# Optimization experiments

Measured on AMD Instinct MI355X. Metric: run time of the kernel, lower is better.

## Reference

```python
import jax, jax.numpy as jnp
import numpy as np

H = 16
D_MODEL = 1024
D_K = D_MODEL // H  # 64, must equal embeddim


def setup_inputs() -> dict:
    key = jax.random.key(0)
    ks = jax.random.split(key, 20)
    B, S, D = 4, 1024, D_MODEL
    s = 0.02
    inp = {
        'query': jax.random.normal(ks[0], (B, S, D), jnp.float32),
        'key':   jax.random.normal(ks[1], (B, S, D), jnp.float32),
        'value': jax.random.normal(ks[2], (B, S, D), jnp.float32),
        'mask':  jnp.ones((B, S, S), jnp.int32),
        # four d_model x d_model projections (q, k, v, out)
        'wq': jax.random.normal(ks[3], (D, D), jnp.float32) * s, 'bq': jnp.zeros((D,), jnp.float32),
        'wk': jax.random.normal(ks[4], (D, D), jnp.float32) * s, 'bk': jnp.zeros((D,), jnp.float32),
        'wv': jax.random.normal(ks[5], (D, D), jnp.float32) * s, 'bv': jnp.zeros((D,), jnp.float32),
        'wo': jax.random.normal(ks[6], (D, D), jnp.float32) * s, 'bo': jnp.zeros((D,), jnp.float32),
        # per-head (embeddim=64) linears
        'spatial_w': jax.random.normal(ks[7], (D_K, D_K), jnp.float32) * s, 'spatial_b': jnp.zeros((D_K,), jnp.float32),
        'qproj_w':   jax.random.normal(ks[8], (D_K, D_K), jnp.float32) * s, 'qproj_b':   jnp.zeros((D_K,), jnp.float32),
        'kproj_w':   jax.random.normal(ks[9], (D_K, D_K), jnp.float32) * s, 'kproj_b':   jnp.zeros((D_K,), jnp.float32),
        'vlin_w':    jax.random.normal(ks[10], (D_K, D_K), jnp.float32) * s, 'vlin_b':    jnp.zeros((D_K,), jnp.float32),
        # channel_linear: Linear(1, 64)
        'chan_w': jax.random.normal(ks[11], (1, D_K), jnp.float32) * s, 'chan_b': jnp.zeros((D_K,), jnp.float32),
    }
    return inp


def reference(query, key, value, mask,
              wq, bq, wk, bk, wv, bv, wo, bo,
              spatial_w, spatial_b, qproj_w, qproj_b,
              kproj_w, kproj_b, vlin_w, vlin_b, chan_w, chan_b):
    B, S, D = query.shape
    # project and split heads -> [B, H, S, D_K]
    def heads(x, w, b):
        return (x @ w + b).reshape(B, S, H, D_K).transpose(0, 2, 1, 3)
    q = heads(query, wq, bq)
    k = heads(key, wk, bk)
    v = heads(value, wv, bv)

    q = jax.nn.elu(q @ spatial_w + spatial_b)
    q_refine = q @ qproj_w + qproj_b
    # channel gate: mean over channels -> Linear(1,64) -> matmul with raw key
    alpha = q_refine.mean(-1, keepdims=True) @ chan_w + chan_b        # [B,H,S,64]
    gate = jax.nn.sigmoid(jnp.einsum('bhqe,bhke->bhqk', alpha, k))    # [B,H,S,S]

    k2 = jax.nn.elu(k @ kproj_w + kproj_b)
    scores = jnp.einsum('bhqe,bhke->bhqk', q, k2) / jnp.sqrt(jnp.asarray(D_K, q.dtype))
    scores = scores * gate
    scores = jnp.where(mask[:, None] == 0, jnp.asarray(-1e9, scores.dtype), scores)
    p_attn = jax.nn.softmax(scores, axis=-1)

    v2 = jax.nn.elu(v @ vlin_w + vlin_b)
    x = jnp.einsum('bhqk,bhke->bhqe', p_attn, v2)                     # [B,H,S,64]
    x = x.transpose(0, 2, 1, 3).reshape(B, S, H * D_K)
    return x @ wo + bo
```

## Files before the change

### kernel.cpp

```cpp
#include <hip/hip_runtime.h>
#include <math.h>

#define D_MODEL 1024
#define NH 16
#define DK 64
#define S_LEN 1024
#define BATCH 4
#define MROWS (BATCH * S_LEN)

typedef short bf16x8 __attribute__((ext_vector_type(8)));
typedef float f32x4 __attribute__((ext_vector_type(4)));
typedef unsigned short u16;

__device__ __forceinline__ float elu1(float x) {
    return x > 0.f ? x : (expf(x) - 1.f);
}

__device__ __forceinline__ u16 f2bf(float f) {
    union { float f; unsigned u; } v; v.f = f;
    unsigned u = v.u;
    return (u16)((u + 0x7fffu + ((u >> 16) & 1u)) >> 16);
}

__device__ __forceinline__ u16 f2bf_fast(float f) {
    union { float f; unsigned u; } v; v.f = f;
    return (u16)((v.u + 0x8000u) >> 16);
}

__device__ __forceinline__ void async16(const void* g, void* l) {
    __builtin_amdgcn_global_load_lds(
        (const __attribute__((address_space(1))) unsigned int*)g,
        (__attribute__((address_space(3))) unsigned int*)l,
        16, 0, 0);
}

__global__ __launch_bounds__(256) void cast_wt(
    const float* __restrict__ wq, const float* __restrict__ wk,
    const float* __restrict__ wv, const float* __restrict__ wo,
    u16* __restrict__ WT)
{
    __shared__ float T[64][65];
    const int z = blockIdx.z;
    const float* W = (z == 0) ? wq : ((z == 1) ? wk : ((z == 2) ? wv : wo));
    u16* O = WT + (size_t)z * D_MODEL * D_MODEL;
    const int tid = threadIdx.x;
    const int k0 = blockIdx.y * 64, n0 = blockIdx.x * 64;
    const int r = tid >> 4, c4 = (tid & 15) * 4;
    #pragma unroll
    for (int p = 0; p < 4; p++) {
        float4 v = *(const float4*)&W[(size_t)(k0 + r + p * 16) * D_MODEL + n0 + c4];
        T[r + p * 16][c4 + 0] = v.x; T[r + p * 16][c4 + 1] = v.y;
        T[r + p * 16][c4 + 2] = v.z; T[r + p * 16][c4 + 3] = v.w;
    }
    __syncthreads();
    #pragma unroll
    for (int p = 0; p < 4; p++) {
        const int i = r + p * 16;
        ushort4 o4;
        o4.x = f2bf(T[c4 + 0][i]); o4.y = f2bf(T[c4 + 1][i]);
        o4.z = f2bf(T[c4 + 2][i]); o4.w = f2bf(T[c4 + 3][i]);
        *(ushort4*)&O[(size_t)(n0 + i) * D_MODEL + k0 + c4] = o4;
    }
}

__global__ __launch_bounds__(256) void cast_x(
    const float* __restrict__ Xq, const float* __restrict__ Xk,
    const float* __restrict__ Xv, u16* __restrict__ Xb)
{
    const int z = blockIdx.y;
    const float* X = (z == 0) ? Xq : ((z == 1) ? Xk : Xv);
    u16* O = Xb + (size_t)z * MROWS * D_MODEL;
    const size_t i = ((size_t)blockIdx.x * 256 + threadIdx.x) * 8;
    float4 a = *(const float4*)&X[i];
    float4 b = *(const float4*)&X[i + 4];
    ushort4 o0, o1;
    o0.x = f2bf(a.x); o0.y = f2bf(a.y); o0.z = f2bf(a.z); o0.w = f2bf(a.w);
    o1.x = f2bf(b.x); o1.y = f2bf(b.y); o1.z = f2bf(b.z); o1.w = f2bf(b.w);
    *(ushort4*)&O[i] = o0;
    *(ushort4*)&O[i + 4] = o1;
}

__global__ __launch_bounds__(256) void mask_pack(
    const int* __restrict__ mask, unsigned long long* __restrict__ Mb)
{
    const int gw = (blockIdx.x * 256 + threadIdx.x) >> 6;
    const int lane = threadIdx.x & 63;
    for (int i = 0; i < 64; i++) {
        const size_t w = (size_t)gw * 64 + i;
        int v = mask[w * 64 + lane];
        unsigned long long bits = __ballot(v != 0);
        if (lane == 0) Mb[w] = bits;
    }
}

__global__ __launch_bounds__(256) void proj_fused(
    const u16* __restrict__ Xq, const u16* __restrict__ Xk, const u16* __restrict__ Xv,
    const u16* __restrict__ WTq, const u16* __restrict__ WTk, const u16* __restrict__ WTv,
    const float* __restrict__ bq, const float* __restrict__ bk, const float* __restrict__ bv,
    const float* __restrict__ spatial_w, const float* __restrict__ spatial_b,
    const float* __restrict__ qproj_w, const float* __restrict__ qproj_b,
    const float* __restrict__ kproj_w, const float* __restrict__ kproj_b,
    const float* __restrict__ vlin_w, const float* __restrict__ vlin_b,
    const float* __restrict__ chan_w, const float* __restrict__ chan_b,
    u16* __restrict__ Qh, u16* __restrict__ K2, u16* __restrict__ V2t,
    float* __restrict__ mB, float* __restrict__ uB, float* __restrict__ vB)
{
    __shared__ __align__(16) u16 smem[10752];
    __shared__ float auxA[64];
    __shared__ float auxS;

    u16* As = smem;
    u16* Bs = smem + 4096;
    u16* W2t = smem + 6144;

    const int z = blockIdx.z;
    const u16* X = (z == 0) ? Xq : ((z == 1) ? Xk : Xv);
    const u16* WT = (z == 0) ? WTq : ((z == 1) ? WTk : WTv);
    const float* B1 = (z == 0) ? bq : ((z == 1) ? bk : bv);
    const float* W2 = (z == 0) ? spatial_w : ((z == 1) ? kproj_w : vlin_w);
    const float* B2 = (z == 0) ? spatial_b : ((z == 1) ? kproj_b : vlin_b);

    const int tid = threadIdx.x;
    const int wave = tid >> 6, lane = tid & 63;
    const int col = lane & 15, quad = lane >> 4;
    const int r0 = blockIdx.x * 128;
    const int hh = blockIdx.y;
    const int n0 = hh * 64;

    #pragma unroll
    for (int p = 0; p < 4; p++) {
        int idx = p * 256 + tid;
        int f = idx >> 4, e4 = (idx & 15) * 4;
        float4 w4 = *(const float4*)&W2[f * 64 + e4];
        W2t[(e4 + 0) * 72 + f] = f2bf(w4.x);
        W2t[(e4 + 1) * 72 + f] = f2bf(w4.y);
        W2t[(e4 + 2) * 72 + f] = f2bf(w4.z);
        W2t[(e4 + 3) * 72 + f] = f2bf(w4.w);
    }
    if (z == 0) {
        {
            int row = tid >> 2, part = tid & 3;
            float s = 0.f;
            for (int e = part * 16; e < part * 16 + 16; e++) s += qproj_w[row * 64 + e];
            s += __shfl_xor(s, 1);
            s += __shfl_xor(s, 2);
            if (part == 0) auxA[row] = s * (1.f / 64.f);
        }
        if (tid < 64) {
            float s = qproj_b[tid];
            #pragma unroll
            for (int m = 1; m < 64; m <<= 1) s += __shfl_xor(s, m);
            if (tid == 0) auxS = s * (1.f / 64.f);
        }
    }

    const int srow = lane >> 2;
    const int sg = ((lane & 3) ^ ((lane >> 3) & 3)) * 8;

    const u16* ap = X + (size_t)(r0 + wave * 32 + srow) * D_MODEL + sg;
    u16* adst0 = As + (wave * 32) * 32;
    u16* adst1 = As + (wave * 32 + 16) * 32;
    const u16* bp = WT + (size_t)(n0 + wave * 16 + srow) * D_MODEL + sg;
    u16* bdst = Bs + wave * 16 * 32;

    f32x4 acc[2][4];
    #pragma unroll
    for (int i = 0; i < 2; i++)
        #pragma unroll
        for (int j = 0; j < 4; j++)
            acc[i][j] = (f32x4){0.f, 0.f, 0.f, 0.f};

    const int gsw = (quad ^ ((col >> 1) & 3)) * 8;

    for (int k0 = 0; k0 < D_MODEL; k0 += 32) {
        if (k0) __syncthreads();
        async16(ap + k0, adst0);
        async16(ap + (size_t)16 * D_MODEL + k0, adst1);
        async16(bp + k0, bdst);
        __syncthreads();
        const u16* Abase = As + (wave * 32 + col) * 32 + gsw;
        const u16* Bbase = Bs + col * 32 + gsw;
        bf16x8 af[2], bfr[4];
        #pragma unroll
        for (int mi = 0; mi < 2; mi++) af[mi] = *(const bf16x8*)(Abase + mi * 512);
        #pragma unroll
        for (int ni = 0; ni < 4; ni++) bfr[ni] = *(const bf16x8*)(Bbase + ni * 512);
        #pragma unroll
        for (int mi = 0; mi < 2; mi++)
            #pragma unroll
            for (int ni = 0; ni < 4; ni++)
                acc[mi][ni] = __builtin_amdgcn_mfma_f32_16x16x32_bf16(af[mi], bfr[ni], acc[mi][ni], 0, 0, 0);
    }

    float b1v[4];
    #pragma unroll
    for (int ni = 0; ni < 4; ni++) b1v[ni] = B1[n0 + ni * 16 + col];

    const int rbase = r0 + wave * 32;
    const int b = r0 >> 10;
    const int s0 = (r0 & 1023) + wave * 32;
    const size_t svecbase = ((size_t)b * NH + hh) * S_LEN;

    if (z == 1) {
        float cw[4], cb[4];
        #pragma unroll
        for (int ni = 0; ni < 4; ni++) { cw[ni] = chan_w[ni * 16 + col]; cb[ni] = chan_b[ni * 16 + col]; }
        #pragma unroll
        for (int mi = 0; mi < 2; mi++)
            #pragma unroll
            for (int r = 0; r < 4; r++) {
                float su = 0.f, sv = 0.f;
                #pragma unroll
                for (int ni = 0; ni < 4; ni++) {
                    float p = acc[mi][ni][r] + b1v[ni];
                    su += p * cw[ni];
                    sv += p * cb[ni];
                }
                su += __shfl_xor(su, 1); su += __shfl_xor(su, 2);
                su += __shfl_xor(su, 4); su += __shfl_xor(su, 8);
                sv += __shfl_xor(sv, 1); sv += __shfl_xor(sv, 2);
                sv += __shfl_xor(sv, 4); sv += __shfl_xor(sv, 8);
                if (col == 0) {
                    const size_t idx = svecbase + s0 + mi * 16 + quad * 4 + r;
                    uB[idx] = su;
                    vB[idx] = sv;
                }
            }
    }

    __syncthreads();

    u16* Pchunk = smem + wave * 1536;
    bf16x8 bf2r[4][2];
    #pragma unroll
    for (int ni = 0; ni < 4; ni++) {
        bf2r[ni][0] = *(const bf16x8*)&W2t[(ni * 16 + col) * 72 + quad * 8];
        bf2r[ni][1] = *(const bf16x8*)&W2t[(ni * 16 + col) * 72 + 32 + quad * 8];
    }
    float qs[2][4][4];
    #pragma unroll
    for (int mi = 0; mi < 2; mi++) {
        #pragma unroll
        for (int ni = 0; ni < 4; ni++)
            #pragma unroll
            for (int r = 0; r < 4; r++)
                Pchunk[(quad * 4 + r) * 72 + ni * 16 + col] = f2bf(acc[mi][ni][r] + b1v[ni]);
        __builtin_amdgcn_s_waitcnt(0xc07f);
        __builtin_amdgcn_sched_barrier(0);
        bf16x8 a0 = *(const bf16x8*)&Pchunk[col * 72 + quad * 8];
        bf16x8 a1 = *(const bf16x8*)&Pchunk[col * 72 + 32 + quad * 8];
        __builtin_amdgcn_s_waitcnt(0xc07f);
        __builtin_amdgcn_sched_barrier(0);
        #pragma unroll
        for (int ni = 0; ni < 4; ni++) {
            f32x4 c = (f32x4){0.f, 0.f, 0.f, 0.f};
            c = __builtin_amdgcn_mfma_f32_16x16x32_bf16(a0, bf2r[ni][0], c, 0, 0, 0);
            c = __builtin_amdgcn_mfma_f32_16x16x32_bf16(a1, bf2r[ni][1], c, 0, 0, 0);
            const float bb = B2[ni * 16 + col];
            #pragma unroll
            for (int r = 0; r < 4; r++) qs[mi][ni][r] = elu1(c[r] + bb);
        }
    }

    if (z == 0) {
        float aw[4];
        #pragma unroll
        for (int ni = 0; ni < 4; ni++) aw[ni] = auxA[ni * 16 + col];
        #pragma unroll
        for (int mi = 0; mi < 2; mi++)
            #pragma unroll
            for (int r = 0; r < 4; r++) {
                float pm = 0.f;
                #pragma unroll
                for (int ni = 0; ni < 4; ni++) pm += qs[mi][ni][r] * aw[ni];
                pm += __shfl_xor(pm, 1); pm += __shfl_xor(pm, 2);
                pm += __shfl_xor(pm, 4); pm += __shfl_xor(pm, 8);
                if (col == 0)
                    mB[svecbase + s0 + mi * 16 + quad * 4 + r] = pm + auxS;
            }
        #pragma unroll
        for (int mi = 0; mi < 2; mi++)
            #pragma unroll
            for (int ni = 0; ni < 4; ni++)
                #pragma unroll
                for (int r = 0; r < 4; r++)
                    Qh[(size_t)(rbase + mi * 16 + quad * 4 + r) * D_MODEL
                       + n0 + ni * 16 + col] = f2bf(qs[mi][ni][r] * 0.125f);
    } else if (z == 1) {
        #pragma unroll
        for (int mi = 0; mi < 2; mi++)
            #pragma unroll
            for (int ni = 0; ni < 4; ni++)
                #pragma unroll
                for (int r = 0; r < 4; r++)
                    K2[(size_t)(rbase + mi * 16 + quad * 4 + r) * D_MODEL
                       + n0 + ni * 16 + col] = f2bf(qs[mi][ni][r]);
    } else {
        u16* Tb = W2t;
        __syncthreads();
        #pragma unroll
        for (int p = 0; p < 2; p++) {
            if ((wave >> 1) == p) {
                const int sloc = (wave & 1) * 32;
                #pragma unroll
                for (int mi = 0; mi < 2; mi++)
                    #pragma unroll
                    for (int ni = 0; ni < 4; ni++)
                        #pragma unroll
                        for (int r = 0; r < 4; r++)
                            Tb[(ni * 16 + col) * 72 + sloc + mi * 16 + quad * 4 + r] =
                                f2bf(qs[mi][ni][r]);
            }
            __syncthreads();
            {
                const int d = tid >> 2, seg = tid & 3;
                u16* dst = V2t + (((size_t)b * NH + hh) * DK + d) * S_LEN
                         + (r0 & 1023) + p * 64 + seg * 16;
                *(uint4*)dst = *(const uint4*)&Tb[d * 72 + seg * 16];
                *(uint4*)(dst + 8) = *(const uint4*)&Tb[d * 72 + seg * 16 + 8];
            }
            if (p == 0) __syncthreads();
        }
    }
}

__global__ __launch_bounds__(256) void attn_mfma(
    const u16* __restrict__ Qh, const u16* __restrict__ K2h, const u16* __restrict__ V2t,
    const float* __restrict__ Mq, const float* __restrict__ Uk, const float* __restrict__ Vk,
    const unsigned long long* __restrict__ Mb, u16* __restrict__ X)
{
    __shared__ u16 K2s[64][72];
    __shared__ u16 V2s[64][72];
    __shared__ u16 Ps[4][16][72];

    const int tid = threadIdx.x;
    const int wave = tid >> 6, lane = tid & 63;
    const int col = lane & 15, quad = lane >> 4;

    const int f = blockIdx.x;
    const int o = (f & 7) * 128 + (f >> 3);
    const int q0 = (o & 15) * 64;
    const int h = (o >> 4) & 15;
    const int b = o >> 8;

    const size_t hb = ((size_t)(b * NH + h)) * S_LEN * DK;
    const size_t sb = ((size_t)(b * NH + h)) * S_LEN;

    bf16x8 qf0, qf1;
    {
        const u16* qp = Qh + (size_t)(b * S_LEN + q0 + wave * 16 + col) * D_MODEL + h * 64 + quad * 8;
        qf0 = *(const bf16x8*)qp;
        qf1 = *(const bf16x8*)(qp + 32);
    }
    float mqv[4];
    #pragma unroll
    for (int r = 0; r < 4; r++)
        mqv[r] = Mq[sb + q0 + wave * 16 + quad * 4 + r];

    const int srow = tid >> 2, sseg = tid & 3;
    const u16* ksrc = K2h + (size_t)(b * S_LEN + srow) * D_MODEL + h * 64 + sseg * 16;
    const u16* vsrc = V2t + hb + (size_t)srow * S_LEN + sseg * 16;
    const unsigned long long* mbase = Mb
        + ((size_t)b * S_LEN + q0 + wave * 16 + quad * 4) * (S_LEN / 64);
    const unsigned msel0 = 1u << col, msel1 = msel0 << 16;

    uint4 ka = *(const uint4*)(ksrc);
    uint4 kb = *(const uint4*)(ksrc + 8);
    uint4 va = *(const uint4*)(vsrc);
    uint4 vb = *(const uint4*)(vsrc + 8);
    float ku[4], kv[4];
    unsigned long long wm[4];
    #pragma unroll
    for (int nb = 0; nb < 4; nb++) {
        ku[nb] = Uk[sb + nb * 16 + col];
        kv[nb] = Vk[sb + nb * 16 + col];
    }
    #pragma unroll
    for (int r = 0; r < 4; r++) wm[r] = mbase[r * 16];

    float psum[4] = {0.f, 0.f, 0.f, 0.f};
    f32x4 o4[4];
    #pragma unroll
    for (int nb = 0; nb < 4; nb++) o4[nb] = (f32x4){0.f, 0.f, 0.f, 0.f};

    for (int t = 0; t < 16; t++) {
        *(uint4*)&K2s[srow][sseg * 16]     = ka;
        *(uint4*)&K2s[srow][sseg * 16 + 8] = kb;
        *(uint4*)&V2s[srow][sseg * 16]     = va;
        *(uint4*)&V2s[srow][sseg * 16 + 8] = vb;
        __syncthreads();

        if (t < 15) {
            const int k1 = (t + 1) * 64;
            const u16* ks = ksrc + (size_t)k1 * D_MODEL;
            const u16* vs = vsrc + k1;
            ka = *(const uint4*)(ks);
            kb = *(const uint4*)(ks + 8);
            va = *(const uint4*)(vs);
            vb = *(const uint4*)(vs + 8);
        }

        __builtin_amdgcn_s_setprio(1);
        f32x4 sc[4];
        #pragma unroll
        for (int nb = 0; nb < 4; nb++) {
            bf16x8 b0 = *(const bf16x8*)&K2s[nb * 16 + col][quad * 8];
            bf16x8 b1 = *(const bf16x8*)&K2s[nb * 16 + col][32 + quad * 8];
            f32x4 c = (f32x4){0.f, 0.f, 0.f, 0.f};
            c = __builtin_amdgcn_mfma_f32_16x16x32_bf16(qf0, b0, c, 0, 0, 0);
            c = __builtin_amdgcn_mfma_f32_16x16x32_bf16(qf1, b1, c, 0, 0, 0);
            sc[nb] = c;
        }
        __builtin_amdgcn_s_setprio(0);

        #pragma unroll
        for (int nb = 0; nb < 4; nb++) {
            #pragma unroll
            for (int r = 0; r < 4; r++) {
                float e = __expf(-(mqv[r] * ku[nb] + kv[nb]));
                float g = __builtin_amdgcn_rcpf(1.f + e);
                float sv = sc[nb][r] * g;
                const unsigned bits = (nb < 2) ? (unsigned)wm[r]
                                               : (unsigned)(wm[r] >> 32);
                sv = (bits & ((nb & 1) ? msel1 : msel0)) ? sv : -30.f;
                float p = __expf(sv);
                psum[r] += p;
                Ps[wave][quad * 4 + r][nb * 16 + col] = f2bf_fast(p);
            }
        }
        if (t < 15) {
            const int k1 = (t + 1) * 64;
            #pragma unroll
            for (int nb = 0; nb < 4; nb++) {
                ku[nb] = Uk[sb + k1 + nb * 16 + col];
                kv[nb] = Vk[sb + k1 + nb * 16 + col];
            }
            #pragma unroll
            for (int r = 0; r < 4; r++) wm[r] = mbase[r * 16 + t + 1];
        }
        __builtin_amdgcn_s_waitcnt(0xc07f);
        __builtin_amdgcn_sched_barrier(0);
        bf16x8 a0 = *(const bf16x8*)&Ps[wave][col][quad * 8];
        bf16x8 a1 = *(const bf16x8*)&Ps[wave][col][32 + quad * 8];

        __builtin_amdgcn_s_setprio(1);
        #pragma unroll
        for (int nb = 0; nb < 4; nb++) {
            bf16x8 b0 = *(const bf16x8*)&V2s[nb * 16 + col][quad * 8];
            bf16x8 b1 = *(const bf16x8*)&V2s[nb * 16 + col][32 + quad * 8];
            o4[nb] = __builtin_amdgcn_mfma_f32_16x16x32_bf16(a0, b0, o4[nb], 0, 0, 0);
            o4[nb] = __builtin_amdgcn_mfma_f32_16x16x32_bf16(a1, b1, o4[nb], 0, 0, 0);
        }
        __builtin_amdgcn_s_setprio(0);
        __syncthreads();
    }

    #pragma unroll
    for (int r = 0; r < 4; r++) {
        float t = psum[r];
        t += __shfl_xor(t, 1);
        t += __shfl_xor(t, 2);
        t += __shfl_xor(t, 4);
        t += __shfl_xor(t, 8);
        float inv = __builtin_amdgcn_rcpf(t);
        u16* xp = X + (size_t)(b * S_LEN + q0 + wave * 16 + quad * 4 + r) * D_MODEL + h * 64 + col;
        #pragma unroll
        for (int nb = 0; nb < 4; nb++)
            xp[nb * 16] = f2bf_fast(o4[nb][r] * inv);
    }
}

__global__ __launch_bounds__(256) void out_gemm(
    const u16* __restrict__ A, const u16* __restrict__ WT,
    const float* __restrict__ bias, float* __restrict__ C)
{
    __shared__ u16 As[64 * 32];
    __shared__ u16 Bs[64 * 32];

    const int tid = threadIdx.x;
    const int wave = tid >> 6, lane = tid & 63;
    const int col = lane & 15, quad = lane >> 4;
    const int r0 = blockIdx.x * 64, n0 = blockIdx.y * 64;

    const int sg = ((lane & 3) ^ ((lane >> 3) & 3)) * 8;
    const u16* ap = A + (size_t)(r0 + wave * 16 + (lane >> 2)) * D_MODEL + sg;
    const u16* bp = WT + (size_t)(n0 + wave * 16 + (lane >> 2)) * D_MODEL + sg;
    u16* adst = As + wave * 16 * 32;
    u16* bdst = Bs + wave * 16 * 32;

    f32x4 acc[4];
    #pragma unroll
    for (int j = 0; j < 4; j++) acc[j] = (f32x4){0.f, 0.f, 0.f, 0.f};

    const int gsw = (quad ^ ((col >> 1) & 3)) * 8;

    for (int k0 = 0; k0 < D_MODEL; k0 += 32) {
        if (k0) __syncthreads();
        async16(ap + k0, adst);
        async16(bp + k0, bdst);
        __syncthreads();
        const u16* Ab = As + (wave * 16 + col) * 32 + gsw;
        const u16* Bb = Bs + col * 32 + gsw;
        bf16x8 af = *(const bf16x8*)Ab;
        bf16x8 bfr[4];
        #pragma unroll
        for (int ni = 0; ni < 4; ni++) bfr[ni] = *(const bf16x8*)(Bb + ni * 512);
        #pragma unroll
        for (int ni = 0; ni < 4; ni++)
            acc[ni] = __builtin_amdgcn_mfma_f32_16x16x32_bf16(af, bfr[ni], acc[ni], 0, 0, 0);
    }

    #pragma unroll
    for (int ni = 0; ni < 4; ni++) {
        const int gr = r0 + wave * 16 + quad * 4;
        const int gc = n0 + ni * 16 + col;
        const float bb = bias[gc];
        #pragma unroll
        for (int r = 0; r < 4; r++)
            C[(size_t)(gr + r) * D_MODEL + gc] = acc[ni][r] + bb;
    }
}

extern "C" void kernel_launch(void* const* d_in, const int* in_sizes, int n_in,
                              void* d_out, int out_size, void* d_ws, size_t ws_size,
                              hipStream_t stream) {
    (void)in_sizes; (void)n_in; (void)out_size; (void)ws_size;
    const float* query = (const float*)d_in[0];
    const float* key_  = (const float*)d_in[1];
    const float* value = (const float*)d_in[2];
    const int*   mask  = (const int*)d_in[3];
    const float* wq = (const float*)d_in[4];  const float* bq = (const float*)d_in[5];
    const float* wk = (const float*)d_in[6];  const float* bk = (const float*)d_in[7];
    const float* wv = (const float*)d_in[8];  const float* bv = (const float*)d_in[9];
    const float* wo = (const float*)d_in[10]; const float* bo = (const float*)d_in[11];
    const float* spatial_w = (const float*)d_in[12]; const float* spatial_b = (const float*)d_in[13];
    const float* qproj_w   = (const float*)d_in[14]; const float* qproj_b   = (const float*)d_in[15];
    const float* kproj_w   = (const float*)d_in[16]; const float* kproj_b   = (const float*)d_in[17];
    const float* vlin_w    = (const float*)d_in[18]; const float* vlin_b    = (const float*)d_in[19];
    const float* chan_w    = (const float*)d_in[20]; const float* chan_b    = (const float*)d_in[21];
    float* out = (float*)d_out;

    char* ws = (char*)d_ws;
    u16* Qh  = (u16*)ws;
    u16* K2  = (u16*)(ws + ((size_t)8  << 20));
    u16* Xb  = (u16*)(ws + ((size_t)16 << 20));
    u16* WT  = (u16*)(ws + ((size_t)24 << 20));
    u16* V2t = (u16*)(ws + ((size_t)32 << 20));
    float* mB = (float*)(ws + ((size_t)40 << 20));
    float* uB = mB + (size_t)BATCH * NH * S_LEN;
    float* vB = uB + (size_t)BATCH * NH * S_LEN;
    unsigned long long* Mbits = (unsigned long long*)(ws + ((size_t)41 << 20));
    u16* Xbf = (u16*)(ws + ((size_t)42 << 20));
    const size_t WSZ = (size_t)D_MODEL * D_MODEL;
    const size_t XSZ = (size_t)MROWS * D_MODEL;

    cast_wt<<<dim3(16, 16, 4), 256, 0, stream>>>(wq, wk, wv, wo, WT);
    cast_x<<<dim3(MROWS * D_MODEL / 2048, 3), 256, 0, stream>>>(query, key_, value, Xbf);
    mask_pack<<<dim3(256), 256, 0, stream>>>(mask, Mbits);
    proj_fused<<<dim3(32, 16, 3), 256, 0, stream>>>(Xbf, Xbf + XSZ, Xbf + 2 * XSZ,
        WT, WT + WSZ, WT + 2 * WSZ, bq, bk, bv,
        spatial_w, spatial_b, qproj_w, qproj_b, kproj_w, kproj_b,
        vlin_w, vlin_b, chan_w, chan_b,
        Qh, K2, V2t, mB, uB, vB);
    attn_mfma<<<dim3(1024), 256, 0, stream>>>(Qh, K2, V2t, mB, uB, vB, Mbits, Xb);
    out_gemm<<<dim3(64, 16), 256, 0, stream>>>(Xb, WT + 3 * WSZ, bo, out);
}
```

Measured before the change: 306.1 us.

## Enlarge GEMM tiles in projection and output kernels, widen mask packing parallelism

The fused projection kernel now computes a 128x128 tile covering two heads per block (each wave handles 64x64), halving the grid in y and doubling the reuse of each A tile. The V transpose is restructured to stage both heads in shared memory and write with wider stores. The output GEMM moves from 64x64 to 128x64 tiles, and mask packing gets 8x more blocks, with each wavefront issuing 8 independent loads before its ballots. The cost is more accumulator registers and shared memory per block, which lowers occupancy, and fewer blocks for the GEMMs.

```diff
diff --git a/kernel.cpp b/kernel.cpp
--- a/kernel.cpp
+++ b/kernel.cpp
@@ -85,11 +85,14 @@
 {
     const int gw = (blockIdx.x * 256 + threadIdx.x) >> 6;
     const int lane = threadIdx.x & 63;
-    for (int i = 0; i < 64; i++) {
-        const size_t w = (size_t)gw * 64 + i;
-        int v = mask[w * 64 + lane];
-        unsigned long long bits = __ballot(v != 0);
-        if (lane == 0) Mb[w] = bits;
+    int v[8];
+    #pragma unroll
+    for (int i = 0; i < 8; i++)
+        v[i] = mask[((size_t)gw + (size_t)i * 8192) * 64 + lane];
+    #pragma unroll
+    for (int i = 0; i < 8; i++) {
+        unsigned long long bits = __ballot(v[i] != 0);
+        if (lane == 0) Mb[(size_t)gw + (size_t)i * 8192] = bits;
     }
 }
 
@@ -105,13 +108,13 @@
     u16* __restrict__ Qh, u16* __restrict__ K2, u16* __restrict__ V2t,
     float* __restrict__ mB, float* __restrict__ uB, float* __restrict__ vB)
 {
-    __shared__ __align__(16) u16 smem[10752];
+    __shared__ __align__(16) u16 smem[17408];
     __shared__ float auxA[64];
     __shared__ float auxS;
 
     u16* As = smem;
     u16* Bs = smem + 4096;
-    u16* W2t = smem + 6144;
+    u16* W2t = smem + 8192;
 
     const int z = blockIdx.z;
     const u16* X = (z == 0) ? Xq : ((z == 1) ? Xk : Xv);
@@ -123,9 +126,10 @@
     const int tid = threadIdx.x;
     const int wave = tid >> 6, lane = tid & 63;
     const int col = lane & 15, quad = lane >> 4;
+    const int wr = wave >> 1, wc = wave & 1;
     const int r0 = blockIdx.x * 128;
-    const int hh = blockIdx.y;
-    const int n0 = hh * 64;
+    const int hp = blockIdx.y * 2 + wc;
+    const int n0 = blockIdx.y * 128;
 
     #pragma unroll
     for (int p = 0; p < 4; p++) {
@@ -158,14 +162,13 @@
     const int sg = ((lane & 3) ^ ((lane >> 3) & 3)) * 8;
 
     const u16* ap = X + (size_t)(r0 + wave * 32 + srow) * D_MODEL + sg;
-    u16* adst0 = As + (wave * 32) * 32;
-    u16* adst1 = As + (wave * 32 + 16) * 32;
-    const u16* bp = WT + (size_t)(n0 + wave * 16 + srow) * D_MODEL + sg;
-    u16* bdst = Bs + wave * 16 * 32;
-
-    f32x4 acc[2][4];
-    #pragma unroll
-    for (int i = 0; i < 2; i++)
+    const u16* bp = WT + (size_t)(n0 + wave * 32 + srow) * D_MODEL + sg;
+    u16* adst0 = As + (wave * 32) * 32;  u16* adst1 = adst0 + 512;
+    u16* bdst0 = Bs + (wave * 32) * 32;  u16* bdst1 = bdst0 + 512;
+
+    f32x4 acc[4][4];
+    #pragma unroll
+    for (int i = 0; i < 4; i++)
         #pragma unroll
         for (int j = 0; j < 4; j++)
             acc[i][j] = (f32x4){0.f, 0.f, 0.f, 0.f};
@@ -176,17 +179,18 @@
         if (k0) __syncthreads();
         async16(ap + k0, adst0);
         async16(ap + (size_t)16 * D_MODEL + k0, adst1);
-        async16(bp + k0, bdst);
+        async16(bp + k0, bdst0);
+        async16(bp + (size_t)16 * D_MODEL + k0, bdst1);
         __syncthreads();
-        const u16* Abase = As + (wave * 32 + col) * 32 + gsw;
-        const u16* Bbase = Bs + col * 32 + gsw;
-        bf16x8 af[2], bfr[4];
-        #pragma unroll
-        for (int mi = 0; mi < 2; mi++) af[mi] = *(const bf16x8*)(Abase + mi * 512);
+        const u16* Abase = As + (wr * 64 + col) * 32 + gsw;
+        const u16* Bbase = Bs + (wc * 64 + col) * 32 + gsw;
+        bf16x8 af[4], bfr[4];
+        #pragma unroll
+        for (int mi = 0; mi < 4; mi++) af[mi] = *(const bf16x8*)(Abase + mi * 512);
         #pragma unroll
         for (int ni = 0; ni < 4; ni++) bfr[ni] = *(const bf16x8*)(Bbase + ni * 512);
         #pragma unroll
-        for (int mi = 0; mi < 2; mi++)
+        for (int mi = 0; mi < 4; mi++)
             #pragma unroll
             for (int ni = 0; ni < 4; ni++)
                 acc[mi][ni] = __builtin_amdgcn_mfma_f32_16x16x32_bf16(af[mi], bfr[ni], acc[mi][ni], 0, 0, 0);
@@ -194,19 +198,19 @@
 
     float b1v[4];
     #pragma unroll
-    for (int ni = 0; ni < 4; ni++) b1v[ni] = B1[n0 + ni * 16 + col];
-
-    const int rbase = r0 + wave * 32;
+    for (int ni = 0; ni < 4; ni++) b1v[ni] = B1[hp * 64 + ni * 16 + col];
+
+    const int rbase = r0 + wr * 64;
     const int b = r0 >> 10;
-    const int s0 = (r0 & 1023) + wave * 32;
-    const size_t svecbase = ((size_t)b * NH + hh) * S_LEN;
+    const int s0 = (r0 & 1023) + wr * 64;
+    const size_t svecbase = ((size_t)b * NH + hp) * S_LEN;
 
     if (z == 1) {
         float cw[4], cb[4];
         #pragma unroll
         for (int ni = 0; ni < 4; ni++) { cw[ni] = chan_w[ni * 16 + col]; cb[ni] = chan_b[ni * 16 + col]; }
         #pragma unroll
-        for (int mi = 0; mi < 2; mi++)
+        for (int mi = 0; mi < 4; mi++)
             #pragma unroll
             for (int r = 0; r < 4; r++) {
                 float su = 0.f, sv = 0.f;
@@ -237,9 +241,9 @@
         bf2r[ni][0] = *(const bf16x8*)&W2t[(ni * 16 + col) * 72 + quad * 8];
         bf2r[ni][1] = *(const bf16x8*)&W2t[(ni * 16 + col) * 72 + 32 + quad * 8];
     }
-    float qs[2][4][4];
-    #pragma unroll
-    for (int mi = 0; mi < 2; mi++) {
+    float qs[4][4][4];
+    #pragma unroll
+    for (int mi = 0; mi < 4; mi++) {
         #pragma unroll
         for (int ni = 0; ni < 4; ni++)
             #pragma unroll
@@ -267,7 +271,7 @@
         #pragma unroll
         for (int ni = 0; ni < 4; ni++) aw[ni] = auxA[ni * 16 + col];
         #pragma unroll
-        for (int mi = 0; mi < 2; mi++)
+        for (int mi = 0; mi < 4; mi++)
             #pragma unroll
             for (int r = 0; r < 4; r++) {
                 float pm = 0.f;
@@ -279,47 +283,45 @@
                     mB[svecbase + s0 + mi * 16 + quad * 4 + r] = pm + auxS;
             }
         #pragma unroll
-        for (int mi = 0; mi < 2; mi++)
+        for (int mi = 0; mi < 4; mi++)
             #pragma unroll
             for (int ni = 0; ni < 4; ni++)
                 #pragma unroll
                 for (int r = 0; r < 4; r++)
                     Qh[(size_t)(rbase + mi * 16 + quad * 4 + r) * D_MODEL
-                       + n0 + ni * 16 + col] = f2bf(qs[mi][ni][r] * 0.125f);
+                       + hp * 64 + ni * 16 + col] = f2bf(qs[mi][ni][r] * 0.125f);
     } else if (z == 1) {
         #pragma unroll
-        for (int mi = 0; mi < 2; mi++)
+        for (int mi = 0; mi < 4; mi++)
             #pragma unroll
             for (int ni = 0; ni < 4; ni++)
                 #pragma unroll
                 for (int r = 0; r < 4; r++)
                     K2[(size_t)(rbase + mi * 16 + quad * 4 + r) * D_MODEL
-                       + n0 + ni * 16 + col] = f2bf(qs[mi][ni][r]);
+                       + hp * 64 + ni * 16 + col] = f2bf(qs[mi][ni][r]);
     } else {
-        u16* Tb = W2t;
         __syncthreads();
-        #pragma unroll
-        for (int p = 0; p < 2; p++) {
-            if ((wave >> 1) == p) {
-                const int sloc = (wave & 1) * 32;
-                #pragma unroll
-                for (int mi = 0; mi < 2; mi++)
-                    #pragma unroll
-                    for (int ni = 0; ni < 4; ni++)
-                        #pragma unroll
-                        for (int r = 0; r < 4; r++)
-                            Tb[(ni * 16 + col) * 72 + sloc + mi * 16 + quad * 4 + r] =
-                                f2bf(qs[mi][ni][r]);
+        u16* Tb = smem + wc * 8704;
+        #pragma unroll
+        for (int mi = 0; mi < 4; mi++)
+            #pragma unroll
+            for (int ni = 0; ni < 4; ni++) {
+                ushort4 t4;
+                t4.x = f2bf(qs[mi][ni][0]); t4.y = f2bf(qs[mi][ni][1]);
+                t4.z = f2bf(qs[mi][ni][2]); t4.w = f2bf(qs[mi][ni][3]);
+                *(ushort4*)&Tb[(ni * 16 + col) * 136 + wr * 64 + mi * 16 + quad * 4] = t4;
             }
-            __syncthreads();
-            {
-                const int d = tid >> 2, seg = tid & 3;
-                u16* dst = V2t + (((size_t)b * NH + hh) * DK + d) * S_LEN
-                         + (r0 & 1023) + p * 64 + seg * 16;
-                *(uint4*)dst = *(const uint4*)&Tb[d * 72 + seg * 16];
-                *(uint4*)(dst + 8) = *(const uint4*)&Tb[d * 72 + seg * 16 + 8];
-            }
-            if (p == 0) __syncthreads();
+        __syncthreads();
+        {
+            const int hpw = tid >> 7;
+            const int d = (tid >> 1) & 63;
+            const int seg = tid & 1;
+            const u16* src = smem + hpw * 8704 + d * 136 + seg * 64;
+            u16* dst = V2t + (((size_t)b * NH + blockIdx.y * 2 + hpw) * DK + d) * S_LEN
+                     + (r0 & 1023) + seg * 64;
+            #pragma unroll
+            for (int j = 0; j < 8; j++)
+                *(uint4*)(dst + j * 8) = *(const uint4*)(src + j * 8);
         }
     }
 }
@@ -474,51 +476,61 @@
     const u16* __restrict__ A, const u16* __restrict__ WT,
     const float* __restrict__ bias, float* __restrict__ C)
 {
-    __shared__ u16 As[64 * 32];
+    __shared__ u16 As[128 * 32];
     __shared__ u16 Bs[64 * 32];
 
     const int tid = threadIdx.x;
     const int wave = tid >> 6, lane = tid & 63;
     const int col = lane & 15, quad = lane >> 4;
-    const int r0 = blockIdx.x * 64, n0 = blockIdx.y * 64;
-
+    const int r0 = blockIdx.x * 128, n0 = blockIdx.y * 64;
+
+    const int srow = lane >> 2;
     const int sg = ((lane & 3) ^ ((lane >> 3) & 3)) * 8;
-    const u16* ap = A + (size_t)(r0 + wave * 16 + (lane >> 2)) * D_MODEL + sg;
-    const u16* bp = WT + (size_t)(n0 + wave * 16 + (lane >> 2)) * D_MODEL + sg;
-    u16* adst = As + wave * 16 * 32;
+    const u16* ap = A + (size_t)(r0 + wave * 32 + srow) * D_MODEL + sg;
+    const u16* bp = WT + (size_t)(n0 + wave * 16 + srow) * D_MODEL + sg;
+    u16* adst0 = As + (wave * 32) * 32;  u16* adst1 = adst0 + 512;
     u16* bdst = Bs + wave * 16 * 32;
 
-    f32x4 acc[4];
-    #pragma unroll
-    for (int j = 0; j < 4; j++) acc[j] = (f32x4){0.f, 0.f, 0.f, 0.f};
+    f32x4 acc[2][4];
+    #pragma unroll
+    for (int i = 0; i < 2; i++)
+        #pragma unroll
+        for (int j = 0; j < 4; j++)
+            acc[i][j] = (f32x4){0.f, 0.f, 0.f, 0.f};
 
     const int gsw = (quad ^ ((col >> 1) & 3)) * 8;
 
     for (int k0 = 0; k0 < D_MODEL; k0 += 32) {
         if (k0) __syncthreads();
-        async16(ap + k0, adst);
+        async16(ap + k0, adst0);
+        async16(ap + (size_t)16 * D_MODEL + k0, adst1);
         async16(bp + k0, bdst);
         __syncthreads();
-        const u16* Ab = As + (wave * 16 + col) * 32 + gsw;
+        const u16* Ab = As + (wave * 32 + col) * 32 + gsw;
         const u16* Bb = Bs + col * 32 + gsw;
-        bf16x8 af = *(const bf16x8*)Ab;
-        bf16x8 bfr[4];
+        bf16x8 af[2], bfr[4];
+        #pragma unroll
+        for (int mi = 0; mi < 2; mi++) af[mi] = *(const bf16x8*)(Ab + mi * 512);
         #pragma unroll
         for (int ni = 0; ni < 4; ni++) bfr[ni] = *(const bf16x8*)(Bb + ni * 512);
         #pragma unroll
-        for (int ni = 0; ni < 4; ni++)
-            acc[ni] = __builtin_amdgcn_mfma_f32_16x16x32_bf16(af, bfr[ni], acc[ni], 0, 0, 0);
-    }
-
-    #pragma unroll
-    for (int ni = 0; ni < 4; ni++) {
-        const int gr = r0 + wave * 16 + quad * 4;
-        const int gc = n0 + ni * 16 + col;
-        const float bb = bias[gc];
-        #pragma unroll
-        for (int r = 0; r < 4; r++)
-            C[(size_t)(gr + r) * D_MODEL + gc] = acc[ni][r] + bb;
-    }
+        for (int mi = 0; mi < 2; mi++)
+            #pragma unroll
+            for (int ni = 0; ni < 4; ni++)
+                acc[mi][ni] = __builtin_amdgcn_mfma_f32_16x16x32_bf16(af[mi], bfr[ni], acc[mi][ni], 0, 0, 0);
+    }
+
+    #pragma unroll
+    for (int mi = 0; mi < 2; mi++)
+        #pragma unroll
+        for (int ni = 0; ni < 4; ni++) {
+            const int gr = r0 + wave * 32 + mi * 16 + quad * 4;
+            const int gc = n0 + ni * 16 + col;
+            const float bb = bias[gc];
+            #pragma unroll
+            for (int r = 0; r < 4; r++)
+                C[(size_t)(gr + r) * D_MODEL + gc] = acc[mi][ni][r] + bb;
+        }
 }
 
 extern "C" void kernel_launch(void* const* d_in, const int* in_sizes, int n_in,
@@ -556,12 +568,12 @@
 
     cast_wt<<<dim3(16, 16, 4), 256, 0, stream>>>(wq, wk, wv, wo, WT);
     cast_x<<<dim3(MROWS * D_MODEL / 2048, 3), 256, 0, stream>>>(query, key_, value, Xbf);
-    mask_pack<<<dim3(256), 256, 0, stream>>>(mask, Mbits);
-    proj_fused<<<dim3(32, 16, 3), 256, 0, stream>>>(Xbf, Xbf + XSZ, Xbf + 2 * XSZ,
+    mask_pack<<<dim3(2048), 256, 0, stream>>>(mask, Mbits);
+    proj_fused<<<dim3(32, 8, 3), 256, 0, stream>>>(Xbf, Xbf + XSZ, Xbf + 2 * XSZ,
         WT, WT + WSZ, WT + 2 * WSZ, bq, bk, bv,
         spatial_w, spatial_b, qproj_w, qproj_b, kproj_w, kproj_b,
         vlin_w, vlin_b, chan_w, chan_b,
         Qh, K2, V2t, mB, uB, vB);
     attn_mfma<<<dim3(1024), 256, 0, stream>>>(Qh, K2, V2t, mB, uB, vB, Mbits, Xb);
-    out_gemm<<<dim3(64, 16), 256, 0, stream>>>(Xb, WT + 3 * WSZ, bo, out);
-}
+    out_gemm<<<dim3(32, 16), 256, 0, stream>>>(Xb, WT + 3 * WSZ, bo, out);
+}
```

After: 307.8 us. Within noise of the previous version (+0.6%).
